# Performance work log

Hardware: AMD Instinct MI355X
Metric: run time of the kernel (lower is better)

## Reference

```python
import jax, jax.numpy as jnp
import numpy as np

IN_F = 1024
OUT_F = 1024
GRID = 8
TOKENS = 8192


def setup_inputs() -> dict:
    key = jax.random.key(0)
    k_x, k_w, k_b, k_s = jax.random.split(key, 4)
    x = jax.random.normal(k_x, (TOKENS, IN_F), dtype=jnp.float32)
    # kaiming_uniform_(nonlinearity='linear'): bound = sqrt(3/fan_in)
    bound_w = float(np.sqrt(3.0 / IN_F))
    W = jax.random.uniform(k_w, (OUT_F, IN_F), minval=-bound_w, maxval=bound_w, dtype=jnp.float32)
    # nn.Linear default bias init: U(-1/sqrt(fan_in), 1/sqrt(fan_in))
    bound_b = float(1.0 / np.sqrt(IN_F))
    b = jax.random.uniform(k_b, (OUT_F,), minval=-bound_b, maxval=bound_b, dtype=jnp.float32)
    spline_weight = jax.random.uniform(k_s, (OUT_F, IN_F, GRID), minval=-0.1, maxval=0.1, dtype=jnp.float32)
    grid = jnp.linspace(-3.0, 3.0, GRID, dtype=jnp.float32)
    return {"x": x, "W": W, "b": b, "spline_weight": spline_weight, "grid": grid}


def reference(x, W, b, spline_weight, grid):
    grid_size = spline_weight.shape[-1]
    # base path: Linear(silu(x))
    base = jnp.einsum('ti,oi->to', jax.nn.silu(x), W) + b
    # RBF basis: [tokens, in_features, grid_size]
    denom = 2.0 / (grid_size - 1) + 1e-05
    basis = jnp.exp(-(((x[..., None] - grid) / denom) ** 2))
    spline = jnp.einsum('tig,oig->to', basis, spline_weight)
    return base + spline
```

## Files before the change

### kernel.cpp

```cpp
#include <hip/hip_runtime.h>
#include <hip/hip_bf16.h>

#define IN_F   1024
#define OUT_F  1024
#define TOKENS 8192
#define KTOT   9216
#define KHALF  4608
#define NTILE  72

typedef __attribute__((ext_vector_type(8))) short  bf16x8;
typedef __attribute__((ext_vector_type(4))) float  f32x4;

template<int M> struct ModeT { static constexpr int value = M; };

__device__ __forceinline__ unsigned int f2bf(float f) {
    union { float f; unsigned int u; } v; v.f = f;
    unsigned int r = v.u + 0x7fffu + ((v.u >> 16) & 1u);
    return r >> 16;
}

__device__ __forceinline__ void prep_a_body(int idx, const float* __restrict__ x,
                                            const float* __restrict__ grid,
                                            unsigned short* __restrict__ A)
{
    int t = idx >> 10;
    int i = idx & 1023;
    float xv = x[idx];
    float sil = xv / (1.0f + __expf(-xv));
    A[(size_t)t * KTOT + i] = (unsigned short)f2bf(sil);

    const float invd = 1.0f / (2.0f / 7.0f + 1e-5f);
    unsigned int h[8];
    #pragma unroll
    for (int g = 0; g < 8; ++g) {
        float d = (xv - grid[g]) * invd;
        h[g] = f2bf(__expf(-d * d));
    }
    uint4 pk;
    pk.x = h[0] | (h[1] << 16);
    pk.y = h[2] | (h[3] << 16);
    pk.z = h[4] | (h[5] << 16);
    pk.w = h[6] | (h[7] << 16);
    *reinterpret_cast<uint4*>(&A[(size_t)t * KTOT + IN_F + (size_t)i * 8]) = pk;
}

__device__ __forceinline__ void prep_b_body(int idx, const float* __restrict__ W,
                                            const float* __restrict__ spl,
                                            unsigned short* __restrict__ B)
{
    int o  = idx / (KTOT / 8);
    int c8 = idx - o * (KTOT / 8);
    const float* src = (c8 < IN_F / 8)
        ? (W   + (size_t)o * IN_F     + (size_t)c8 * 8)
        : (spl + (size_t)o * IN_F * 8 + (size_t)(c8 - IN_F / 8) * 8);
    const float4* s4 = reinterpret_cast<const float4*>(src);
    float4 lo = s4[0], hi = s4[1];
    uint4 pk;
    pk.x = f2bf(lo.x) | (f2bf(lo.y) << 16);
    pk.y = f2bf(lo.z) | (f2bf(lo.w) << 16);
    pk.z = f2bf(hi.x) | (f2bf(hi.y) << 16);
    pk.w = f2bf(hi.z) | (f2bf(hi.w) << 16);
    *reinterpret_cast<uint4*>(&B[(size_t)o * KTOT + (size_t)c8 * 8]) = pk;
}

__global__ __launch_bounds__(256)
void prep_fused(const float* __restrict__ x, const float* __restrict__ grid,
                const float* __restrict__ W, const float* __restrict__ spl,
                unsigned short* __restrict__ A, unsigned short* __restrict__ B)
{
    int b = blockIdx.x;
    if (b < (TOKENS * IN_F) / 256)
        prep_a_body(b * 256 + threadIdx.x, x, grid, A);
    else
        prep_b_body((b - (TOKENS * IN_F) / 256) * 256 + threadIdx.x, W, spl, B);
}

__global__ __launch_bounds__(256)
void prep_a_kernel(const float* __restrict__ x, const float* __restrict__ grid,
                   unsigned short* __restrict__ A)
{
    prep_a_body(blockIdx.x * blockDim.x + threadIdx.x, x, grid, A);
}

__global__ __launch_bounds__(256)
void prep_b_kernel(const float* __restrict__ W, const float* __restrict__ spl,
                   unsigned short* __restrict__ B)
{
    prep_b_body(blockIdx.x * blockDim.x + threadIdx.x, W, spl, B);
}

#define GLOAD(src, dst) __builtin_amdgcn_global_load_lds( \
    (const __attribute__((address_space(1))) void*)(src),  \
    (__attribute__((address_space(3))) void*)(dst), 16, 0, 0)
#define SBAR()  __builtin_amdgcn_s_barrier()
#define SCH0()  __builtin_amdgcn_sched_barrier(0)
#define VMC0()  asm volatile("s_waitcnt vmcnt(0)" ::: "memory")
#define SGB(m, n) __builtin_amdgcn_sched_group_barrier((m), (n), 0)

__global__ __launch_bounds__(512, 2)
void gemm_kan2(const unsigned short* __restrict__ A,
               const unsigned short* __restrict__ B,
               float* __restrict__ P, int rows)
{
    __shared__ char lds[131072];

    const int bid  = blockIdx.x;
    const int sk   = bid & 1;
    const int bn   = (bid >> 1) & 3;
    const int bm   = bid >> 3;
    const int tid  = threadIdx.x;
    const int wave = tid >> 6, lane = tid & 63;
    const int wr   = wave >> 2, wc = wave & 3;
    const int fr   = lane & 15, kg = lane >> 4;
    const int sw   = fr & 7;
    const int koff[2] = { (kg ^ sw) * 16, ((4 | kg) ^ sw) * 16 };
    const int k0 = sk * KHALF;

    const int trow = tid >> 3;
    const int ksrc = ((tid & 7) ^ (trow & 7)) * 8;
    const unsigned short* gA = A + (size_t)(bm * 256 + trow) * KTOT + k0 + ksrc;
    const unsigned short* gB = B + (size_t)(bn * 256 + trow) * KTOT + k0 + ksrc;
    const size_t R64 = (size_t)64 * KTOT;

    f32x4 acc[8][4];
    const f32x4 zero = {0.f, 0.f, 0.f, 0.f};
    #pragma unroll
    for (int m = 0; m < 8; ++m)
        #pragma unroll
        for (int n = 0; n < 4; ++n) acc[m][n] = zero;

    {
        char* dA = lds + tid * 16;
        char* dB = lds + 65536 + tid * 16;
        GLOAD(gA,           dA);           GLOAD(gA + R64,     dA + 8192);
        GLOAD(gA + 2 * R64, dA + 16384);   GLOAD(gA + 3 * R64, dA + 24576);
        GLOAD(gB,           dB);           GLOAD(gB + R64,     dB + 8192);
        GLOAD(gB + 2 * R64, dB + 16384);   GLOAD(gB + 3 * R64, dB + 24576);
        gA += 64; gB += 64;
    }
    VMC0(); SBAR(); SCH0();

    const int aOff = (wr * 64 + fr) * 128;
    const int bOff = (wc * 32 + fr) * 128;

    bf16x8 af[4][2], bfLo[2][2], bfHi[2][2];
    int u = 0;

    auto tile = [&](auto mC) {
        constexpr int MODE = decltype(mC)::value;
        char* bufA = lds + (u & 1) * 32768;
        char* bufB = lds + 65536 + (u & 1) * 32768;

        #pragma unroll
        for (int mi = 0; mi < 4; ++mi)
            #pragma unroll
            for (int ks = 0; ks < 2; ++ks)
                af[mi][ks] = *(const bf16x8*)(bufA + aOff + mi * 2048 + koff[ks]);
        #pragma unroll
        for (int ni = 0; ni < 2; ++ni)
            #pragma unroll
            for (int ks = 0; ks < 2; ++ks)
                bfLo[ni][ks] = *(const bf16x8*)(bufB + bOff + ni * 2048 + koff[ks]);

        __builtin_amdgcn_s_setprio(1);

        #pragma unroll
        for (int mi = 0; mi < 4; ++mi)
            #pragma unroll
            for (int ni = 0; ni < 2; ++ni)
                #pragma unroll
                for (int ks = 0; ks < 2; ++ks)
                    acc[mi][ni] = __builtin_amdgcn_mfma_f32_16x16x32_bf16(
                        af[mi][ks], bfLo[ni][ks], acc[mi][ni], 0, 0, 0);

        #pragma unroll
        for (int ni = 0; ni < 2; ++ni)
            #pragma unroll
            for (int ks = 0; ks < 2; ++ks)
                bfHi[ni][ks] = *(const bf16x8*)(bufB + bOff + 16384 + ni * 2048 + koff[ks]);

        #pragma unroll
        for (int mi = 0; mi < 4; ++mi)
            #pragma unroll
            for (int ni = 0; ni < 2; ++ni)
                #pragma unroll
                for (int ks = 0; ks < 2; ++ks)
                    acc[mi][2 + ni] = __builtin_amdgcn_mfma_f32_16x16x32_bf16(
                        af[mi][ks], bfHi[ni][ks], acc[mi][2 + ni], 0, 0, 0);

        #pragma unroll
        for (int mi = 0; mi < 4; ++mi)
            #pragma unroll
            for (int ks = 0; ks < 2; ++ks)
                af[mi][ks] = *(const bf16x8*)(bufA + aOff + 16384 + mi * 2048 + koff[ks]);

        if constexpr (MODE == 0) {
            char* dA = lds + ((u & 1) ^ 1) * 32768 + tid * 16;
            char* dB = lds + 65536 + ((u & 1) ^ 1) * 32768 + tid * 16;
            GLOAD(gA,           dA);           GLOAD(gA + R64,     dA + 8192);
            GLOAD(gA + 2 * R64, dA + 16384);   GLOAD(gA + 3 * R64, dA + 24576);
            GLOAD(gB,           dB);           GLOAD(gB + R64,     dB + 8192);
            GLOAD(gB + 2 * R64, dB + 16384);   GLOAD(gB + 3 * R64, dB + 24576);
            gA += 64; gB += 64;
        }

        #pragma unroll
        for (int mi = 0; mi < 4; ++mi)
            #pragma unroll
            for (int ni = 0; ni < 2; ++ni)
                #pragma unroll
                for (int ks = 0; ks < 2; ++ks)
                    acc[4 + mi][ni] = __builtin_amdgcn_mfma_f32_16x16x32_bf16(
                        af[mi][ks], bfLo[ni][ks], acc[4 + mi][ni], 0, 0, 0);

        #pragma unroll
        for (int mi = 0; mi < 4; ++mi)
            #pragma unroll
            for (int ni = 0; ni < 2; ++ni)
                #pragma unroll
                for (int ks = 0; ks < 2; ++ks)
                    acc[4 + mi][2 + ni] = __builtin_amdgcn_mfma_f32_16x16x32_bf16(
                        af[mi][ks], bfHi[ni][ks], acc[4 + mi][2 + ni], 0, 0, 0);

        __builtin_amdgcn_s_setprio(0);

        SGB(0x100, 12);
        #pragma unroll
        for (int i = 0; i < 12; ++i) { SGB(0x8, 2); SGB(0x100, 1); }
        if constexpr (MODE == 0) {
            #pragma unroll
            for (int i = 0; i < 8; ++i) { SGB(0x8, 2); SGB(0x30, 1); }
        } else {
            SGB(0x8, 16);
        }
        SGB(0x8, 24);

        if constexpr (MODE == 0) {
            VMC0();
            SBAR(); SCH0();
        }
    };

    for (u = 0; u < NTILE - 1; ++u) tile(ModeT<0>{});
    tile(ModeT<1>{});

    float* Pp = P + (size_t)sk * rows * OUT_F;
    const size_t orow0 = (size_t)bm * 256 + (size_t)wr * 64;
    const int    ocol0 = bn * 256 + wc * 32;
    #pragma unroll
    for (int n = 0; n < 4; ++n) {
        const int col = ocol0 + (n & 1) * 16 + (n >> 1) * 128 + fr;
        #pragma unroll
        for (int m = 0; m < 8; ++m) {
            const size_t r0 = orow0 + (m & 3) * 16 + (m >> 2) * 128 + kg * 4;
            #pragma unroll
            for (int j = 0; j < 4; ++j)
                Pp[(r0 + j) * OUT_F + col] = acc[m][n][j];
        }
    }
}

__global__ __launch_bounds__(256)
void reduce_kan(const float* __restrict__ P, const float* __restrict__ bias,
                float* __restrict__ out, int n4, int skStride4)
{
    const float4* p0 = (const float4*)P;
    const float4* p1 = p0 + skStride4;
    const float4* bv = (const float4*)bias;
    float4* o = (float4*)out;
    for (int i = blockIdx.x * blockDim.x + threadIdx.x; i < n4;
         i += gridDim.x * blockDim.x) {
        float4 a = p0[i], b = p1[i], c = bv[i & 255];
        float4 r;
        r.x = a.x + b.x + c.x;  r.y = a.y + b.y + c.y;
        r.z = a.z + b.z + c.z;  r.w = a.w + b.w + c.w;
        o[i] = r;
    }
}

extern "C" void kernel_launch(void* const* d_in, const int* in_sizes, int n_in,
                              void* d_out, int out_size, void* d_ws, size_t ws_size,
                              hipStream_t stream)
{
    const float* x    = (const float*)d_in[0];
    const float* W    = (const float*)d_in[1];
    const float* bias = (const float*)d_in[2];
    const float* spl  = (const float*)d_in[3];
    const float* grid = (const float*)d_in[4];
    float* out = (float*)d_out;

    unsigned short* Bw = (unsigned short*)d_ws;
    unsigned short* Aw = Bw + (size_t)OUT_F * KTOT;

    const size_t bBytes = (size_t)OUT_F * KTOT * 2;
    size_t avail = ws_size > bBytes ? ws_size - bBytes : 0;
    long maxRows = (long)(avail / 26624);
    int chunk = (maxRows >= TOKENS) ? TOKENS : (int)((maxRows / 256) * 256);
    if (chunk < 256) chunk = 256;
    float* Pp = (float*)(Aw + (size_t)chunk * KTOT);

    if (chunk == TOKENS) {
        prep_fused<<<(TOKENS * IN_F) / 256 + (OUT_F * (KTOT / 8)) / 256,
                     256, 0, stream>>>(x, grid, W, spl, Aw, Bw);
        gemm_kan2<<<(TOKENS >> 8) * 8, 512, 0, stream>>>(Aw, Bw, Pp, TOKENS);
        int n4 = TOKENS * 256;
        reduce_kan<<<2048, 256, 0, stream>>>(Pp, bias, out, n4, n4);
    } else {
        prep_b_kernel<<<(OUT_F * (KTOT / 8)) / 256, 256, 0, stream>>>(W, spl, Bw);
        for (int t0 = 0; t0 < TOKENS; t0 += chunk) {
            int rows = (TOKENS - t0 < chunk) ? (TOKENS - t0) : chunk;
            prep_a_kernel<<<(rows * IN_F) / 256, 256, 0, stream>>>(
                x + (size_t)t0 * IN_F, grid, Aw);
            gemm_kan2<<<(rows >> 8) * 8, 512, 0, stream>>>(Aw, Bw, Pp, rows);
            int n4 = rows * 256;
            int rblocks = (n4 + 255) / 256; if (rblocks > 2048) rblocks = 2048;
            reduce_kan<<<rblocks, 256, 0, stream>>>(
                Pp, bias, out + (size_t)t0 * OUT_F, n4, n4);
        }
    }
}
```

Baseline: 200.8 us.

## Remap GEMM blocks per XCD and restructure tile instruction schedule

Block indices are remapped so that consecutive blocks, which land round-robin on different XCDs, share the same bm row panel within an XCD. The aim is better L2 reuse of A and B tiles. The per-tile schedule is also reordered: all B fragment LDS reads and the next-tile global-to-LDS loads are issued up front, fenced by sched barriers, and the fine-grained sched_group_barrier interleaving is replaced by per-block setprio wrapping. This may reduce L2 misses and simplify the schedule, but it loses the explicit interleaving of LDS reads with MFMAs.

```diff
diff --git a/kernel.cpp b/kernel.cpp
--- a/kernel.cpp
+++ b/kernel.cpp
@@ -95,7 +95,6 @@
 #define SBAR()  __builtin_amdgcn_s_barrier()
 #define SCH0()  __builtin_amdgcn_sched_barrier(0)
 #define VMC0()  asm volatile("s_waitcnt vmcnt(0)" ::: "memory")
-#define SGB(m, n) __builtin_amdgcn_sched_group_barrier((m), (n), 0)
 
 __global__ __launch_bounds__(512, 2)
 void gemm_kan2(const unsigned short* __restrict__ A,
@@ -105,9 +104,11 @@
     __shared__ char lds[131072];
 
     const int bid  = blockIdx.x;
-    const int sk   = bid & 1;
-    const int bn   = (bid >> 1) & 3;
-    const int bm   = bid >> 3;
+    const int xcd  = bid & 7;
+    const int j    = bid >> 3;
+    const int sk   = j & 1;
+    const int bn   = (j >> 1) & 3;
+    const int bm   = (j >> 3) * 8 + xcd;
     const int tid  = threadIdx.x;
     const int wave = tid >> 6, lane = tid & 63;
     const int wr   = wave >> 2, wc = wave & 3;
@@ -159,40 +160,10 @@
         #pragma unroll
         for (int ni = 0; ni < 2; ++ni)
             #pragma unroll
-            for (int ks = 0; ks < 2; ++ks)
+            for (int ks = 0; ks < 2; ++ks) {
                 bfLo[ni][ks] = *(const bf16x8*)(bufB + bOff + ni * 2048 + koff[ks]);
-
-        __builtin_amdgcn_s_setprio(1);
-
-        #pragma unroll
-        for (int mi = 0; mi < 4; ++mi)
-            #pragma unroll
-            for (int ni = 0; ni < 2; ++ni)
-                #pragma unroll
-                for (int ks = 0; ks < 2; ++ks)
-                    acc[mi][ni] = __builtin_amdgcn_mfma_f32_16x16x32_bf16(
-                        af[mi][ks], bfLo[ni][ks], acc[mi][ni], 0, 0, 0);
-
-        #pragma unroll
-        for (int ni = 0; ni < 2; ++ni)
-            #pragma unroll
-            for (int ks = 0; ks < 2; ++ks)
                 bfHi[ni][ks] = *(const bf16x8*)(bufB + bOff + 16384 + ni * 2048 + koff[ks]);
-
-        #pragma unroll
-        for (int mi = 0; mi < 4; ++mi)
-            #pragma unroll
-            for (int ni = 0; ni < 2; ++ni)
-                #pragma unroll
-                for (int ks = 0; ks < 2; ++ks)
-                    acc[mi][2 + ni] = __builtin_amdgcn_mfma_f32_16x16x32_bf16(
-                        af[mi][ks], bfHi[ni][ks], acc[mi][2 + ni], 0, 0, 0);
-
-        #pragma unroll
-        for (int mi = 0; mi < 4; ++mi)
-            #pragma unroll
-            for (int ks = 0; ks < 2; ++ks)
-                af[mi][ks] = *(const bf16x8*)(bufA + aOff + 16384 + mi * 2048 + koff[ks]);
+            }
 
         if constexpr (MODE == 0) {
             char* dA = lds + ((u & 1) ^ 1) * 32768 + tid * 16;
@@ -203,7 +174,37 @@
             GLOAD(gB + 2 * R64, dB + 16384);   GLOAD(gB + 3 * R64, dB + 24576);
             gA += 64; gB += 64;
         }
-
+        SCH0();
+
+        __builtin_amdgcn_s_setprio(1);
+        #pragma unroll
+        for (int mi = 0; mi < 4; ++mi)
+            #pragma unroll
+            for (int ni = 0; ni < 2; ++ni)
+                #pragma unroll
+                for (int ks = 0; ks < 2; ++ks)
+                    acc[mi][ni] = __builtin_amdgcn_mfma_f32_16x16x32_bf16(
+                        af[mi][ks], bfLo[ni][ks], acc[mi][ni], 0, 0, 0);
+        __builtin_amdgcn_s_setprio(0);
+
+        __builtin_amdgcn_s_setprio(1);
+        #pragma unroll
+        for (int mi = 0; mi < 4; ++mi)
+            #pragma unroll
+            for (int ni = 0; ni < 2; ++ni)
+                #pragma unroll
+                for (int ks = 0; ks < 2; ++ks)
+                    acc[mi][2 + ni] = __builtin_amdgcn_mfma_f32_16x16x32_bf16(
+                        af[mi][ks], bfHi[ni][ks], acc[mi][2 + ni], 0, 0, 0);
+        __builtin_amdgcn_s_setprio(0);
+
+        #pragma unroll
+        for (int mi = 0; mi < 4; ++mi)
+            #pragma unroll
+            for (int ks = 0; ks < 2; ++ks)
+                af[mi][ks] = *(const bf16x8*)(bufA + aOff + 16384 + mi * 2048 + koff[ks]);
+
+        __builtin_amdgcn_s_setprio(1);
         #pragma unroll
         for (int mi = 0; mi < 4; ++mi)
             #pragma unroll
@@ -212,7 +213,9 @@
                 for (int ks = 0; ks < 2; ++ks)
                     acc[4 + mi][ni] = __builtin_amdgcn_mfma_f32_16x16x32_bf16(
                         af[mi][ks], bfLo[ni][ks], acc[4 + mi][ni], 0, 0, 0);
-
+        __builtin_amdgcn_s_setprio(0);
+
+        __builtin_amdgcn_s_setprio(1);
         #pragma unroll
         for (int mi = 0; mi < 4; ++mi)
             #pragma unroll
@@ -221,20 +224,9 @@
                 for (int ks = 0; ks < 2; ++ks)
                     acc[4 + mi][2 + ni] = __builtin_amdgcn_mfma_f32_16x16x32_bf16(
                         af[mi][ks], bfHi[ni][ks], acc[4 + mi][2 + ni], 0, 0, 0);
-
         __builtin_amdgcn_s_setprio(0);
 
-        SGB(0x100, 12);
-        #pragma unroll
-        for (int i = 0; i < 12; ++i) { SGB(0x8, 2); SGB(0x100, 1); }
-        if constexpr (MODE == 0) {
-            #pragma unroll
-            for (int i = 0; i < 8; ++i) { SGB(0x8, 2); SGB(0x30, 1); }
-        } else {
-            SGB(0x8, 16);
-        }
-        SGB(0x8, 24);
-
+        SCH0();
         if constexpr (MODE == 0) {
             VMC0();
             SBAR(); SCH0();
@@ -254,8 +246,8 @@
         for (int m = 0; m < 8; ++m) {
             const size_t r0 = orow0 + (m & 3) * 16 + (m >> 2) * 128 + kg * 4;
             #pragma unroll
-            for (int j = 0; j < 4; ++j)
-                Pp[(r0 + j) * OUT_F + col] = acc[m][n][j];
+            for (int j2 = 0; j2 < 4; ++j2)
+                Pp[(r0 + j2) * OUT_F + col] = acc[m][n][j2];
         }
     }
 }
```

New measurement: 199.1 us. Within noise of the previous version (-0.9%).
